# Kernel optimization log

Measured on AMD Instinct MI355X. Metric: run time of the kernel, lower is better.

The kernel has to match this reference:

```python
import jax, jax.numpy as jnp
import numpy as np

N_NODES = 50000
N_EDGES = 800000
DIM = 256
DEPTH = 4
N_REL = 4
EPS = 1e-5


def setup_inputs() -> dict:
    key = jax.random.key(0)
    ks = jax.random.split(key, 8)
    scale = 1.0 / np.sqrt(DIM)
    return {
        "node_embedding": jax.random.normal(ks[0], (N_NODES, DIM), jnp.float32),
        "weights": jax.random.normal(ks[1], (DEPTH, N_REL, DIM, DIM), jnp.float32) * scale,
        "roots": jax.random.normal(ks[2], (DEPTH, DIM, DIM), jnp.float32) * scale,
        "biases": jax.random.normal(ks[3], (DEPTH, DIM), jnp.float32) * 0.01,
        "ln_gamma": jnp.ones((DEPTH, DIM), jnp.float32),
        "ln_beta": jnp.zeros((DEPTH, DIM), jnp.float32),
        "edge_index": jax.random.randint(ks[4], (2, N_EDGES), 0, N_NODES, jnp.int32),
        "edge_type": jax.random.randint(ks[5], (N_EDGES,), 0, N_REL, jnp.int32),
    }


def _rgcn_layer(X, W, root, bias, gamma, beta, src, dst, etype, inv_deg):
    # RGCNConv with aggr='mean': per-relation transform, then per-relation mean
    # over incoming edges at the target node, summed across relations.
    h = jnp.einsum('ni,rio->rno', X, W)            # [R, N, D]
    msg = h[etype, src] * inv_deg[:, None]         # [E, D] gather + per-relation 1/deg
    agg = jax.ops.segment_sum(msg, dst, num_segments=X.shape[0])  # [N, D]
    out = agg + X @ root + bias
    # LayerNorm
    mu = jnp.mean(out, axis=-1, keepdims=True)
    var = jnp.mean(jnp.square(out - mu), axis=-1, keepdims=True)
    out = (out - mu) * jax.lax.rsqrt(var + EPS) * gamma + beta
    out = jax.nn.elu(out)
    return out + X  # residual connection (dropout p=0 -> identity)


def reference(node_embedding, weights, roots, biases, ln_gamma, ln_beta, edge_index, edge_type):
    src, dst = edge_index[0], edge_index[1]
    # per-(node, relation) in-degree for the relation-wise mean aggregation
    cnt = jnp.zeros((node_embedding.shape[0], N_REL), node_embedding.dtype)
    cnt = cnt.at[dst, edge_type].add(1.0)
    inv_deg = 1.0 / jnp.maximum(cnt[dst, edge_type], 1.0)  # [E]
    X = node_embedding
    for l in range(DEPTH):
        X = _rgcn_layer(X, weights[l], roots[l], biases[l], ln_gamma[l], ln_beta[l],
                        src, dst, edge_type, inv_deg)
    return X
```

## Files before the change

### kernel.cpp

```cpp
#include <hip/hip_runtime.h>
#include <hip/hip_bf16.h>
#include <stdint.h>

#define NN 50000
#define NE 800000
#define DD 256
#define NL 4
#define NRL 4
#define KT 1280
#define KA 1024

typedef float f32x4 __attribute__((ext_vector_type(4)));
typedef __bf16 bf16x8 __attribute__((ext_vector_type(8)));
typedef __bf16 bf16x4 __attribute__((ext_vector_type(4)));
typedef unsigned short u16x4 __attribute__((ext_vector_type(4)));

static __device__ __forceinline__ unsigned short f2bf(float f) {
  __bf16 h = (__bf16)f;
  return __builtin_bit_cast(unsigned short, h);
}

static __device__ __forceinline__ u16x4 pk4(f32x4 v) {
  u16x4 o;
  o.x = f2bf(v.x); o.y = f2bf(v.y); o.z = f2bf(v.z); o.w = f2bf(v.w);
  return o;
}

static __device__ __forceinline__ void async16(const void* g, void* l) {
  __builtin_amdgcn_global_load_lds(
      (const __attribute__((address_space(1))) unsigned int*)g,
      (__attribute__((address_space(3))) unsigned int*)l, 16, 0, 0);
}

static __device__ __forceinline__ void async16nt(const void* g, void* l) {
  __builtin_amdgcn_global_load_lds(
      (const __attribute__((address_space(1))) unsigned int*)g,
      (__attribute__((address_space(3))) unsigned int*)l, 16, 0, 2);
}


__global__ __launch_bounds__(256) void k_hist(const int* __restrict__ ei,
                                              const int* __restrict__ et,
                                              int* __restrict__ cntNR) {
  int e = blockIdx.x * 256 + threadIdx.x;
  if (e >= NE) return;
  int dst = ei[NE + e];
  int r = et[e];
  atomicAdd(&cntNR[dst * 4 + r], 1);
}

__global__ __launch_bounds__(256) void k_scan1(const int* __restrict__ cntNR,
                                               int* __restrict__ offs,
                                               int* __restrict__ bsum) {
  __shared__ int sd[256];
  const int t = threadIdx.x;
  const int n = blockIdx.x * 256 + t;
  int deg = 0;
  if (n < NN) {
    const int* c = cntNR + n * 4;
    deg = c[0] + c[1] + c[2] + c[3];
  }
  sd[t] = deg;
  __syncthreads();
  int val = deg;
  for (int d = 1; d < 256; d <<= 1) {
    int other = (t >= d) ? sd[t - d] : 0;
    __syncthreads();
    val += other;
    sd[t] = val;
    __syncthreads();
  }
  if (n < NN) offs[n] = val - deg;
  if (t == 255) bsum[blockIdx.x] = val;
}

__global__ __launch_bounds__(256) void k_scan2(const int* __restrict__ bsum,
                                               int* __restrict__ boff, int nb) {
  __shared__ int sd[256];
  const int t = threadIdx.x;
  int v = (t < nb) ? bsum[t] : 0;
  sd[t] = v;
  __syncthreads();
  int val = v;
  for (int d = 1; d < 256; d <<= 1) {
    int other = (t >= d) ? sd[t - d] : 0;
    __syncthreads();
    val += other;
    sd[t] = val;
    __syncthreads();
  }
  boff[t] = val - v;
}

__global__ __launch_bounds__(256) void k_scan3(int* __restrict__ offs,
                                               const int* __restrict__ boff,
                                               int* __restrict__ cursor) {
  int n = blockIdx.x * 256 + threadIdx.x;
  if (n < NN) {
    int o = offs[n] + boff[blockIdx.x];
    offs[n] = o;
    cursor[n] = o;
  }
  if (n == 0) offs[NN] = NE;
}

__global__ __launch_bounds__(256) void k_scatter(const int* __restrict__ ei,
                                                 const int* __restrict__ et,
                                                 int* __restrict__ cursor,
                                                 uint32_t* __restrict__ packed) {
  int e = blockIdx.x * 256 + threadIdx.x;
  if (e >= NE) return;
  int src = ei[e];
  int dst = ei[NE + e];
  int r = et[e];
  int pos = atomicAdd(&cursor[dst], 1);
  packed[pos] = (uint32_t)src | ((uint32_t)r << 16);
}

__global__ __launch_bounds__(256) void k_wconv(const float* __restrict__ weights,
                                               const float* __restrict__ roots,
                                               __hip_bfloat16* __restrict__ WbigT) {
  int idx = blockIdx.x * 256 + threadIdx.x;
  if (idx >= NL * DD * KT) return;
  int l = idx / (DD * KT);
  int rem = idx - l * (DD * KT);
  int o = rem / KT;
  int k = rem - o * KT;
  float v;
  if (k < NRL * DD) {
    int r = k >> 8, i = k & 255;
    v = weights[(((size_t)(l * NRL + r) * DD) + i) * DD + o];
  } else {
    int i = k - NRL * DD;
    v = roots[((size_t)l * DD + i) * DD + o];
  }
  WbigT[idx] = __float2bfloat16(v);
}

__global__ __launch_bounds__(256) void k_cast(const float* __restrict__ X,
                                              __hip_bfloat16* __restrict__ Xbf) {
  int i = blockIdx.x * 256 + threadIdx.x;
  if (i >= NN * 64) return;
  const f32x4* Xv = (const f32x4*)X;
  ((u16x4*)Xbf)[i] = pk4(Xv[i]);
}


__global__ __launch_bounds__(256) void k_agg(const __hip_bfloat16* __restrict__ Xbf,
                                             const uint32_t* __restrict__ packed,
                                             const int* __restrict__ offs,
                                             const int* __restrict__ cntNR,
                                             __hip_bfloat16* __restrict__ Abig) {
  const int wid = (blockIdx.x * 256 + threadIdx.x) >> 6;
  const int lane = threadIdx.x & 63;
  if (wid >= NN) return;
  const int beg = offs[wid];
  const int end = offs[wid + 1];
  const bf16x4* __restrict__ Xv = (const bf16x4*)Xbf;

  f32x4 a0 = {0.f, 0.f, 0.f, 0.f}, a1 = a0, a2 = a0, a3 = a0;

  for (int e = beg; e < end; e += 8) {
    uint32_t pv[8];
    bf16x4 vv[8];
#pragma unroll
    for (int i = 0; i < 8; ++i) {
      int ee = e + i;
      ee = (ee < end) ? ee : (end - 1);
      pv[i] = packed[ee];
    }
#pragma unroll
    for (int i = 0; i < 8; ++i) {
      vv[i] = Xv[(int)(pv[i] & 0xFFFFu) * 64 + lane];
    }
    const int nv = end - e;
#pragma unroll
    for (int i = 0; i < 8; ++i) {
      if (i < nv) {
        int r = (int)(pv[i] >> 16);
        f32x4 v = {(float)vv[i][0], (float)vv[i][1], (float)vv[i][2], (float)vv[i][3]};
        if (r == 0) a0 += v;
        else if (r == 1) a1 += v;
        else if (r == 2) a2 += v;
        else a3 += v;
      }
    }
  }

  const int* c = cntNR + wid * 4;
  int c0 = c[0], c1 = c[1], c2 = c[2], c3 = c[3];
  float s0 = 1.0f / (float)(c0 > 1 ? c0 : 1);
  float s1 = 1.0f / (float)(c1 > 1 ? c1 : 1);
  float s2 = 1.0f / (float)(c2 > 1 ? c2 : 1);
  float s3 = 1.0f / (float)(c3 > 1 ? c3 : 1);

  u16x4* Arow = (u16x4*)(Abig + (size_t)wid * KA);
  __builtin_nontemporal_store(pk4(a0 * s0), Arow + 0 * 64 + lane);
  __builtin_nontemporal_store(pk4(a1 * s1), Arow + 1 * 64 + lane);
  __builtin_nontemporal_store(pk4(a2 * s2), Arow + 2 * 64 + lane);
  __builtin_nontemporal_store(pk4(a3 * s3), Arow + 3 * 64 + lane);
}


__global__ __launch_bounds__(256) void k_gemm(const __hip_bfloat16* __restrict__ A,
                                              const __hip_bfloat16* __restrict__ Xbf_in,
                                              const __hip_bfloat16* __restrict__ Bt,
                                              const float* __restrict__ bias,
                                              const float* __restrict__ gamma,
                                              const float* __restrict__ beta,
                                              const float* __restrict__ Xin,
                                              float* __restrict__ Xout,
                                              __hip_bfloat16* __restrict__ Xbf_out) {
  __shared__ __align__(16) char sA[128 * 64];
  __shared__ __align__(16) char sB[256 * 64];
  __shared__ float sRed[128][4];

  const int tid = threadIdx.x;
  const int w = tid >> 6;
  const int lane = tid & 63;
  const int wm = w >> 1, wn = w & 1;
  const int quad = lane >> 4, l15 = lane & 15;
  const int mBase = blockIdx.x * 128;

  const int srow = lane >> 2;
  const int kc = (lane & 3) ^ ((lane >> 3) & 3);

  int am0 = mBase + w * 32 + srow;
  int am1 = am0 + 16;
  if (am0 >= NN) am0 = NN - 1;
  if (am1 >= NN) am1 = NN - 1;
  const char* agp0 = (const char*)A + (size_t)am0 * (KA * 2) + kc * 16;
  const char* agp1 = (const char*)A + (size_t)am1 * (KA * 2) + kc * 16;
  const char* agx0 = (const char*)Xbf_in + (size_t)am0 * (DD * 2) + kc * 16;
  const char* agx1 = (const char*)Xbf_in + (size_t)am1 * (DD * 2) + kc * 16;
  const char* bgp0 = (const char*)Bt + (size_t)(w * 64 + 0 + srow) * (KT * 2) + kc * 16;
  const char* bgp1 = (const char*)Bt + (size_t)(w * 64 + 16 + srow) * (KT * 2) + kc * 16;
  const char* bgp2 = (const char*)Bt + (size_t)(w * 64 + 32 + srow) * (KT * 2) + kc * 16;
  const char* bgp3 = (const char*)Bt + (size_t)(w * 64 + 48 + srow) * (KT * 2) + kc * 16;
  char* alp0 = sA + w * 2048;
  char* alp1 = sA + w * 2048 + 1024;
  char* blp0 = sB + w * 4096 + 0;
  char* blp1 = sB + w * 4096 + 1024;
  char* blp2 = sB + w * 4096 + 2048;
  char* blp3 = sB + w * 4096 + 3072;

  f32x4 acc[4][8];
#pragma unroll
  for (int i = 0; i < 4; ++i)
#pragma unroll
    for (int j = 0; j < 8; ++j) acc[i][j] = (f32x4){0.f, 0.f, 0.f, 0.f};

  const int aslot = (quad ^ ((l15 >> 1) & 3)) * 16;
  const char* aAddr = sA + (wm * 64 + l15) * 64 + aslot;
  const char* bAddr = sB + (wn * 128 + l15) * 64 + aslot;

  for (int k0 = 0; k0 < KT * 2; k0 += 64) {
    __syncthreads();
    if (k0 < KA * 2) {
      async16nt(agp0 + k0, alp0);
      async16nt(agp1 + k0, alp1);
    } else {
      const int kx = k0 - KA * 2;
      async16(agx0 + kx, alp0);
      async16(agx1 + kx, alp1);
    }
    async16(bgp0 + k0, blp0);
    async16(bgp1 + k0, blp1);
    async16(bgp2 + k0, blp2);
    async16(bgp3 + k0, blp3);
    __syncthreads();
    bf16x8 a0 = *(const bf16x8*)(aAddr + 0 * 1024);
    bf16x8 a1 = *(const bf16x8*)(aAddr + 1 * 1024);
    bf16x8 a2 = *(const bf16x8*)(aAddr + 2 * 1024);
    bf16x8 a3 = *(const bf16x8*)(aAddr + 3 * 1024);
#pragma unroll
    for (int nt = 0; nt < 8; ++nt) {
      bf16x8 b = *(const bf16x8*)(bAddr + nt * 1024);
      acc[0][nt] = __builtin_amdgcn_mfma_f32_16x16x32_bf16(a0, b, acc[0][nt], 0, 0, 0);
      acc[1][nt] = __builtin_amdgcn_mfma_f32_16x16x32_bf16(a1, b, acc[1][nt], 0, 0, 0);
      acc[2][nt] = __builtin_amdgcn_mfma_f32_16x16x32_bf16(a2, b, acc[2][nt], 0, 0, 0);
      acc[3][nt] = __builtin_amdgcn_mfma_f32_16x16x32_bf16(a3, b, acc[3][nt], 0, 0, 0);
    }
  }

  float bv[8], gv[8], bev[8];
#pragma unroll
  for (int nt = 0; nt < 8; ++nt) {
    int n = wn * 128 + nt * 16 + l15;
    bv[nt] = bias[n];
    gv[nt] = gamma[n];
    bev[nt] = beta[n];
  }

#pragma unroll
  for (int mt = 0; mt < 4; ++mt) {
#pragma unroll
    for (int reg = 0; reg < 4; ++reg) {
      float s = 0.f, q = 0.f;
#pragma unroll
      for (int nt = 0; nt < 8; ++nt) {
        float v = acc[mt][nt][reg] + bv[nt];
        acc[mt][nt][reg] = v;
        s += v;
        q += v * v;
      }
#pragma unroll
      for (int d = 1; d < 16; d <<= 1) {
        s += __shfl_xor(s, d, 64);
        q += __shfl_xor(q, d, 64);
      }
      if (l15 == 0) {
        int row = wm * 64 + mt * 16 + quad * 4 + reg;
        sRed[row][wn * 2] = s;
        sRed[row][wn * 2 + 1] = q;
      }
    }
  }
  __syncthreads();

#pragma unroll
  for (int mt = 0; mt < 4; ++mt) {
#pragma unroll
    for (int reg = 0; reg < 4; ++reg) {
      int row = wm * 64 + mt * 16 + quad * 4 + reg;
      float ts = sRed[row][0] + sRed[row][2];
      float tq = sRed[row][1] + sRed[row][3];
      float mean = ts * (1.0f / 256.0f);
      float var = tq * (1.0f / 256.0f) - mean * mean;
      float rstd = rsqrtf(var + 1e-5f);
      int m = mBase + row;
      if (m < NN) {
#pragma unroll
        for (int nt = 0; nt < 8; ++nt) {
          int n = wn * 128 + nt * 16 + l15;
          float v = (acc[mt][nt][reg] - mean) * rstd * gv[nt] + bev[nt];
          v = v > 0.0f ? v : (__expf(v) - 1.0f);
          float res = v + Xin[(size_t)m * 256 + n];
          Xout[(size_t)m * 256 + n] = res;
          Xbf_out[(size_t)m * 256 + n] = __float2bfloat16(res);
        }
      }
    }
  }
}


extern "C" void kernel_launch(void* const* d_in, const int* in_sizes, int n_in,
                              void* d_out, int out_size, void* d_ws, size_t ws_size,
                              hipStream_t stream) {
  const float* X0 = (const float*)d_in[0];
  const float* weights = (const float*)d_in[1];
  const float* roots = (const float*)d_in[2];
  const float* biases = (const float*)d_in[3];
  const float* ln_g = (const float*)d_in[4];
  const float* ln_b = (const float*)d_in[5];
  const int* eidx = (const int*)d_in[6];
  const int* etyp = (const int*)d_in[7];
  float* out = (float*)d_out;

  char* ws = (char*)d_ws;
  size_t off = 0;
  auto alloc = [&](size_t bytes) -> char* {
    char* p = ws + off;
    off = (off + bytes + 255) & ~(size_t)255;
    return p;
  };
  __hip_bfloat16* Abig = (__hip_bfloat16*)alloc((size_t)NN * KA * 2);
  __hip_bfloat16* WbigT = (__hip_bfloat16*)alloc((size_t)NL * DD * KT * 2);
  float* Xb0 = (float*)alloc((size_t)NN * DD * 4);
  float* Xb1 = (float*)alloc((size_t)NN * DD * 4);
  __hip_bfloat16* Xbf0 = (__hip_bfloat16*)alloc((size_t)NN * DD * 2);
  __hip_bfloat16* Xbf1 = (__hip_bfloat16*)alloc((size_t)NN * DD * 2);
  int* cntNR = (int*)alloc((size_t)NN * 4 * 4);
  int* offs = (int*)alloc((size_t)(NN + 1) * 4);
  int* cursor = (int*)alloc((size_t)NN * 4);
  uint32_t* packed = (uint32_t*)alloc((size_t)NE * 4);
  int* bsum = (int*)alloc(256 * 4);
  int* boff = (int*)alloc(256 * 4);
  (void)ws_size; (void)in_sizes; (void)n_in; (void)out_size;

  (void)hipMemsetAsync(cntNR, 0, (size_t)NN * 16, stream);
  k_hist<<<(NE + 255) / 256, 256, 0, stream>>>(eidx, etyp, cntNR);
  const int NB = (NN + 255) / 256;
  k_scan1<<<NB, 256, 0, stream>>>(cntNR, offs, bsum);
  k_scan2<<<1, 256, 0, stream>>>(bsum, boff, NB);
  k_scan3<<<NB, 256, 0, stream>>>(offs, boff, cursor);
  k_scatter<<<(NE + 255) / 256, 256, 0, stream>>>(eidx, etyp, cursor, packed);
  k_wconv<<<(NL * DD * KT + 255) / 256, 256, 0, stream>>>(weights, roots, WbigT);
  k_cast<<<(NN * 64 + 255) / 256, 256, 0, stream>>>(X0, Xbf0);

  const float* Xin = X0;
  for (int l = 0; l < NL; ++l) {
    float* Xout = (l == NL - 1) ? out : ((l & 1) ? Xb1 : Xb0);
    const __hip_bfloat16* Xbin = (l & 1) ? Xbf1 : Xbf0;
    __hip_bfloat16* Xbout = (l & 1) ? Xbf0 : Xbf1;
    k_agg<<<(NN * 64 + 255) / 256, 256, 0, stream>>>(Xbin, packed, offs, cntNR, Abig);
    k_gemm<<<(NN + 127) / 128, 256, 0, stream>>>(Abig, Xbin,
                                                 WbigT + (size_t)l * DD * KT,
                                                 biases + (size_t)l * DD,
                                                 ln_g + (size_t)l * DD,
                                                 ln_b + (size_t)l * DD, Xin, Xout, Xbout);
    Xin = Xout;
  }
}
```

Before: 965.6 us.

## Triple-buffer GEMM LDS staging and halve M tile to 64 rows

Rewrites the fused GEMM+LayerNorm kernel main loop to use a three-buffer LDS ring with asynchronous prefetch of the next K-step, a partial vmcnt wait and a single barrier per iteration, instead of two barriers around a synchronous load. The M tile is halved from 128 to 64 rows, doubling the number of blocks (782 vs 391), and launch bounds request two blocks per CU. This aims to overlap global loads with MFMA work and raise occupancy across the CUs, at the cost of re-reading the full weight matrix twice as often per row.

```diff
diff --git a/kernel.cpp b/kernel.cpp
--- a/kernel.cpp
+++ b/kernel.cpp
@@ -202,85 +202,90 @@
 }
 
 
-__global__ __launch_bounds__(256) void k_gemm(const __hip_bfloat16* __restrict__ A,
-                                              const __hip_bfloat16* __restrict__ Xbf_in,
-                                              const __hip_bfloat16* __restrict__ Bt,
-                                              const float* __restrict__ bias,
-                                              const float* __restrict__ gamma,
-                                              const float* __restrict__ beta,
-                                              const float* __restrict__ Xin,
-                                              float* __restrict__ Xout,
-                                              __hip_bfloat16* __restrict__ Xbf_out) {
-  __shared__ __align__(16) char sA[128 * 64];
-  __shared__ __align__(16) char sB[256 * 64];
-  __shared__ float sRed[128][4];
+#define GBUF 20480
+#define NTILE 40
+
+__global__ __launch_bounds__(256, 2) void k_gemm(const __hip_bfloat16* __restrict__ A,
+                                                 const __hip_bfloat16* __restrict__ Xbf_in,
+                                                 const __hip_bfloat16* __restrict__ Bt,
+                                                 const float* __restrict__ bias,
+                                                 const float* __restrict__ gamma,
+                                                 const float* __restrict__ beta,
+                                                 const float* __restrict__ Xin,
+                                                 float* __restrict__ Xout,
+                                                 __hip_bfloat16* __restrict__ Xbf_out) {
+  __shared__ __align__(16) char sLDS[3 * GBUF];
+  __shared__ float sRed[64][4];
 
   const int tid = threadIdx.x;
   const int w = tid >> 6;
   const int lane = tid & 63;
   const int wm = w >> 1, wn = w & 1;
   const int quad = lane >> 4, l15 = lane & 15;
-  const int mBase = blockIdx.x * 128;
+  const int mBase = blockIdx.x * 64;
 
   const int srow = lane >> 2;
-  const int kc = (lane & 3) ^ ((lane >> 3) & 3);
-
-  int am0 = mBase + w * 32 + srow;
-  int am1 = am0 + 16;
-  if (am0 >= NN) am0 = NN - 1;
-  if (am1 >= NN) am1 = NN - 1;
-  const char* agp0 = (const char*)A + (size_t)am0 * (KA * 2) + kc * 16;
-  const char* agp1 = (const char*)A + (size_t)am1 * (KA * 2) + kc * 16;
-  const char* agx0 = (const char*)Xbf_in + (size_t)am0 * (DD * 2) + kc * 16;
-  const char* agx1 = (const char*)Xbf_in + (size_t)am1 * (DD * 2) + kc * 16;
+  const int kc = (lane & 3) ^ ((srow >> 1) & 3);
+
+  int am = mBase + w * 16 + srow;
+  if (am >= NN) am = NN - 1;
+  const char* agp = (const char*)A + (size_t)am * (KA * 2) + kc * 16;
+  const char* agx = (const char*)Xbf_in + (size_t)am * (DD * 2) + kc * 16;
   const char* bgp0 = (const char*)Bt + (size_t)(w * 64 + 0 + srow) * (KT * 2) + kc * 16;
   const char* bgp1 = (const char*)Bt + (size_t)(w * 64 + 16 + srow) * (KT * 2) + kc * 16;
   const char* bgp2 = (const char*)Bt + (size_t)(w * 64 + 32 + srow) * (KT * 2) + kc * 16;
   const char* bgp3 = (const char*)Bt + (size_t)(w * 64 + 48 + srow) * (KT * 2) + kc * 16;
-  char* alp0 = sA + w * 2048;
-  char* alp1 = sA + w * 2048 + 1024;
-  char* blp0 = sB + w * 4096 + 0;
-  char* blp1 = sB + w * 4096 + 1024;
-  char* blp2 = sB + w * 4096 + 2048;
-  char* blp3 = sB + w * 4096 + 3072;
-
-  f32x4 acc[4][8];
-#pragma unroll
-  for (int i = 0; i < 4; ++i)
+
+  char* const lA = sLDS + w * 1024;
+  char* const lB = sLDS + 4096 + w * 4096;
+
+  f32x4 acc[2][8];
+#pragma unroll
+  for (int i = 0; i < 2; ++i)
 #pragma unroll
     for (int j = 0; j < 8; ++j) acc[i][j] = (f32x4){0.f, 0.f, 0.f, 0.f};
 
   const int aslot = (quad ^ ((l15 >> 1) & 3)) * 16;
-  const char* aAddr = sA + (wm * 64 + l15) * 64 + aslot;
-  const char* bAddr = sB + (wn * 128 + l15) * 64 + aslot;
-
-  for (int k0 = 0; k0 < KT * 2; k0 += 64) {
-    __syncthreads();
+  const char* const aBase = sLDS + (wm * 32 + l15) * 64 + aslot;
+  const char* const bBase = sLDS + 4096 + (wn * 128 + l15) * 64 + aslot;
+
+  auto STAGE = [&](int buf, int ts) {
+    const int k0 = ts * 64;
+    char* la = lA + buf * GBUF;
+    char* lb = lB + buf * GBUF;
     if (k0 < KA * 2) {
-      async16nt(agp0 + k0, alp0);
-      async16nt(agp1 + k0, alp1);
+      async16nt(agp + k0, la);
     } else {
-      const int kx = k0 - KA * 2;
-      async16(agx0 + kx, alp0);
-      async16(agx1 + kx, alp1);
-    }
-    async16(bgp0 + k0, blp0);
-    async16(bgp1 + k0, blp1);
-    async16(bgp2 + k0, blp2);
-    async16(bgp3 + k0, blp3);
-    __syncthreads();
+      async16(agx + (k0 - KA * 2), la);
+    }
+    async16(bgp0 + k0, lb);
+    async16(bgp1 + k0, lb + 1024);
+    async16(bgp2 + k0, lb + 2048);
+    async16(bgp3 + k0, lb + 3072);
+  };
+
+  STAGE(0, 0);
+  int cb = 0, sb = 1;
+  for (int t = 0; t < NTILE; ++t) {
+    const int ts = (t + 1 < NTILE) ? (t + 1) : (NTILE - 1);
+    STAGE(sb, ts);
+    __builtin_amdgcn_sched_barrier(0);
+    asm volatile("s_waitcnt vmcnt(5)" ::: "memory");
+    __builtin_amdgcn_s_barrier();
+    __builtin_amdgcn_sched_barrier(0);
+
+    const char* aAddr = aBase + cb * GBUF;
+    const char* bAddr = bBase + cb * GBUF;
     bf16x8 a0 = *(const bf16x8*)(aAddr + 0 * 1024);
     bf16x8 a1 = *(const bf16x8*)(aAddr + 1 * 1024);
-    bf16x8 a2 = *(const bf16x8*)(aAddr + 2 * 1024);
-    bf16x8 a3 = *(const bf16x8*)(aAddr + 3 * 1024);
 #pragma unroll
     for (int nt = 0; nt < 8; ++nt) {
       bf16x8 b = *(const bf16x8*)(bAddr + nt * 1024);
       acc[0][nt] = __builtin_amdgcn_mfma_f32_16x16x32_bf16(a0, b, acc[0][nt], 0, 0, 0);
       acc[1][nt] = __builtin_amdgcn_mfma_f32_16x16x32_bf16(a1, b, acc[1][nt], 0, 0, 0);
-      acc[2][nt] = __builtin_amdgcn_mfma_f32_16x16x32_bf16(a2, b, acc[2][nt], 0, 0, 0);
-      acc[3][nt] = __builtin_amdgcn_mfma_f32_16x16x32_bf16(a3, b, acc[3][nt], 0, 0, 0);
-    }
+    }
+    cb = (cb == 2) ? 0 : cb + 1;
+    sb = (sb == 2) ? 0 : sb + 1;
   }
 
   float bv[8], gv[8], bev[8];
@@ -293,7 +298,7 @@
   }
 
 #pragma unroll
-  for (int mt = 0; mt < 4; ++mt) {
+  for (int mt = 0; mt < 2; ++mt) {
 #pragma unroll
     for (int reg = 0; reg < 4; ++reg) {
       float s = 0.f, q = 0.f;
@@ -310,7 +315,7 @@
         q += __shfl_xor(q, d, 64);
       }
       if (l15 == 0) {
-        int row = wm * 64 + mt * 16 + quad * 4 + reg;
+        int row = wm * 32 + mt * 16 + quad * 4 + reg;
         sRed[row][wn * 2] = s;
         sRed[row][wn * 2 + 1] = q;
       }
@@ -319,10 +324,10 @@
   __syncthreads();
 
 #pragma unroll
-  for (int mt = 0; mt < 4; ++mt) {
+  for (int mt = 0; mt < 2; ++mt) {
 #pragma unroll
     for (int reg = 0; reg < 4; ++reg) {
-      int row = wm * 64 + mt * 16 + quad * 4 + reg;
+      int row = wm * 32 + mt * 16 + quad * 4 + reg;
       float ts = sRed[row][0] + sRed[row][2];
       float tq = sRed[row][1] + sRed[row][3];
       float mean = ts * (1.0f / 256.0f);
@@ -395,11 +400,11 @@
     const __hip_bfloat16* Xbin = (l & 1) ? Xbf1 : Xbf0;
     __hip_bfloat16* Xbout = (l & 1) ? Xbf0 : Xbf1;
     k_agg<<<(NN * 64 + 255) / 256, 256, 0, stream>>>(Xbin, packed, offs, cntNR, Abig);
-    k_gemm<<<(NN + 127) / 128, 256, 0, stream>>>(Abig, Xbin,
-                                                 WbigT + (size_t)l * DD * KT,
-                                                 biases + (size_t)l * DD,
-                                                 ln_g + (size_t)l * DD,
-                                                 ln_b + (size_t)l * DD, Xin, Xout, Xbout);
+    k_gemm<<<(NN + 63) / 64, 256, 0, stream>>>(Abig, Xbin,
+                                               WbigT + (size_t)l * DD * KT,
+                                               biases + (size_t)l * DD,
+                                               ln_g + (size_t)l * DD,
+                                               ln_b + (size_t)l * DD, Xin, Xout, Xbout);
     Xin = Xout;
   }
 }
```

Result: no change. 970.9 us (+0.6%).
